# Kernel optimization log

Measured on AMD Instinct MI355X. Metric: run time of the kernel, lower is better.

Reference implementation:

```python
import jax, jax.numpy as jnp
import numpy as np

OBS, ACT, H, B = 128, 32, 64, 32768
TMAX = 8  # max variable-length GRU steps: (15-1)//2+1 == 15//2+1 == 8
CENTER = 7


def gru_last(x_seq, valid, Wih, Whh, bih, bhh):
    """torch nn.GRU cell, masked scan; returns final hidden at each true length.
    x_seq: (B, TMAX, D), valid: (B, TMAX) bool. Gate order r, z, n."""
    Bn = x_seq.shape[0]
    h0 = jnp.zeros((Bn, Whh.shape[1]), x_seq.dtype)

    def step(h, inp):
        xt, vt = inp  # (B, D), (B,)
        gi = xt @ Wih.T + bih
        gh = h @ Whh.T + bhh
        ir, iz, inn = jnp.split(gi, 3, axis=-1)
        hr, hz, hn = jnp.split(gh, 3, axis=-1)
        r = jax.nn.sigmoid(ir + hr)
        zg = jax.nn.sigmoid(iz + hz)
        n = jnp.tanh(inn + r * hn)
        hnew = (1.0 - zg) * n + zg * h
        h = jnp.where(vt[:, None], hnew, h)
        return h, None

    h, _ = jax.lax.scan(step, h0, (jnp.swapaxes(x_seq, 0, 1), valid.T))
    return h


def setup_inputs() -> dict:
    key = jax.random.key(0)
    ks = jax.random.split(key, 20)
    def p(k, shape, s=0.05):
        return jax.random.normal(k, shape, jnp.float32) * s
    D = OBS + ACT
    return dict(
        obs_chunk=jax.random.normal(ks[0], (B, 15, OBS), jnp.float32),
        act_chunk=jax.random.normal(ks[1], (B, 15, ACT), jnp.float32),
        ln_g=jnp.ones((3,), jnp.float32), ln_b=jnp.zeros((3,), jnp.float32),
        dw1=p(ks[2], (16, 3)), db1=jnp.zeros((16,), jnp.float32),
        dw2=p(ks[3], (8, 16)), db2=jnp.zeros((8,), jnp.float32),
        dw3=p(ks[4], (14, 8)), db3=jnp.zeros((14,), jnp.float32),
        Wih_f=p(ks[5], (3 * H, D)), Whh_f=p(ks[6], (3 * H, H)),
        bih_f=jnp.zeros((3 * H,), jnp.float32), bhh_f=jnp.zeros((3 * H,), jnp.float32),
        Wih_b=p(ks[7], (3 * H, D)), Whh_b=p(ks[8], (3 * H, H)),
        bih_b=jnp.zeros((3 * H,), jnp.float32), bhh_b=jnp.zeros((3 * H,), jnp.float32),
        mw1=p(ks[9], (H, 2 * H)), mb1=jnp.zeros((H,), jnp.float32),
        mw2=p(ks[10], (H, H)), mb2=jnp.zeros((H,), jnp.float32),
        mu_w=p(ks[11], (H, H)), mu_b=jnp.zeros((H,), jnp.float32),
        lv_w=p(ks[12], (H, H)), lv_b=jnp.zeros((H,), jnp.float32),
    )


def reference(obs_chunk, act_chunk, ln_g, ln_b, dw1, db1, dw2, db2, dw3, db3,
              Wih_f, Whh_f, bih_f, bhh_f, Wih_b, Whh_b, bih_b, bhh_b,
              mw1, mb1, mw2, mb2, mu_w, mu_b, lv_w, lv_b):
    C = CENTER
    # --- DynamicTimeWindow features ---
    obs_t = obs_chunk[:, C]  # (B, OBS)
    pr = jax.nn.softmax(obs_t, axis=-1)
    entropy = -jnp.sum(pr * jnp.log(pr + 1e-8), axis=-1, keepdims=True)
    diffs = jnp.stack([jnp.linalg.norm(obs_chunk[:, C - k] - obs_chunk[:, C - k - 1], axis=-1)
                       for k in range(3)], axis=1)
    roc = diffs.mean(axis=1, keepdims=True)
    act_prev = act_chunk[:, C - 1]
    md = max(obs_t.shape[-1], act_prev.shape[-1])
    op = jnp.pad(obs_t, ((0, 0), (0, md - obs_t.shape[-1])))
    ap = jnp.pad(act_prev, ((0, 0), (0, md - act_prev.shape[-1])))
    oc = op - op.mean(axis=1, keepdims=True)
    ac = ap - ap.mean(axis=1, keepdims=True)
    denom = (jnp.linalg.norm(oc, axis=1, keepdims=True)
             * jnp.linalg.norm(ac, axis=1, keepdims=True) + 1e-8)
    corr = jnp.sum(oc * ac, axis=1, keepdims=True) / denom
    f = jnp.concatenate([entropy, roc, corr], axis=1)  # (B, 3)
    mean = f.mean(axis=-1, keepdims=True)
    var = f.var(axis=-1, keepdims=True)  # biased, matches torch LayerNorm
    fn = (f - mean) / jnp.sqrt(var + 1e-5) * ln_g + ln_b
    h1 = jax.nn.relu(fn @ dw1.T + db1)
    h2 = jax.nn.relu(h1 @ dw2.T + db2)
    logits = h2 @ dw3.T + db3  # (B, 14)
    widx = jnp.argmax(logits, axis=1)  # test_mode: argmax of softmax == argmax of logits
    wl = widx + 2  # window_len in [2, 15]
    idxs = jnp.arange(15)[None, :]
    start = (C - (wl - 1) // 2)[:, None]
    end = (C + wl // 2 + 1)[:, None]
    mask = ((idxs >= start) & (idxs < end)).astype(obs_chunk.dtype)  # (B, 15)
    x = jnp.concatenate([obs_chunk, act_chunk], axis=-1) * mask[..., None]  # (B, 15, D)
    # --- BiGRU over variable-length windows ---
    len_f = (wl - 1) // 2 + 1  # (B,)
    len_b = wl // 2 + 1
    t = jnp.arange(TMAX)
    idx_f = C - len_f[:, None] + 1 + t[None, :]  # left-aligned forward window
    idx_b = C + len_b[:, None] - 1 - t[None, :]  # reversed backward window
    seq_f = jnp.take_along_axis(x, idx_f[..., None], axis=1)  # (B, 8, D)
    seq_b = jnp.take_along_axis(x, idx_b[..., None], axis=1)
    vf = t[None, :] < len_f[:, None]
    vb = t[None, :] < len_b[:, None]
    h_f = gru_last(seq_f, vf, Wih_f, Whh_f, bih_f, bhh_f)  # (B, H)
    h_b = gru_last(seq_b, vb, Wih_b, Whh_b, bih_b, bhh_b)
    comb = jnp.concatenate([h_f, h_b], axis=1)  # (B, 2H)
    zenc = jax.nn.relu(comb @ mw1.T + mb1) @ mw2.T + mb2
    mu = zenc @ mu_w.T + mu_b
    sigma = jnp.exp(0.5 * (zenc @ lv_w.T + lv_b))
    z = mu  # test_mode=True
    return (z, mu, sigma)
```

## Files before the change

kernel.cpp:

```cpp
#include <hip/hip_runtime.h>

#define OBS 128
#define ACTD 32
#define DIMX 160
#define HID 64
#define NBATCH 32768
#define TMAXX 8
#define CTR 7
#define NPOS 15

typedef short bf16x8 __attribute__((ext_vector_type(8)));
typedef float f32x4 __attribute__((ext_vector_type(4)));

#define MFMA(a,b,c) __builtin_amdgcn_mfma_f32_16x16x32_bf16((a),(b),(c),0,0,0)

#define CTRL_BYTE 262144
#define SIDX_BYTE 278528
#define SIDX_CAP  66560
#define WB_BYTE   544768
#define COMB_BYTE 757760
#define NCB 64
#define EPB 512
#define HEAD_W_OFF 10752
#define TOTAL_SLOTS 13312

__device__ __forceinline__ unsigned short f2bf(float f) {
  unsigned u = __float_as_uint(f);
  return (unsigned short)((u + 0x7FFFu + ((u >> 16) & 1u)) >> 16);
}
__device__ __forceinline__ unsigned cvtpk(float a, float b) {
  unsigned r;
  asm("v_cvt_pk_bf16_f32 %0, %1, %2" : "=v"(r) : "v"(a), "v"(b));
  return r;
}

__device__ __forceinline__ float wsum(float v) {
#pragma unroll
  for (int s = 1; s < 64; s <<= 1) v += __shfl_xor(v, s);
  return v;
}
__device__ __forceinline__ float wmax(float v) {
#pragma unroll
  for (int s = 1; s < 64; s <<= 1) v = fmaxf(v, __shfl_xor(v, s));
  return v;
}

__global__ __launch_bounds__(256) void k_prep(
    const float* __restrict__ Wih_f, const float* __restrict__ Whh_f,
    const float* __restrict__ Wih_b, const float* __restrict__ Whh_b,
    const float* __restrict__ mw1, const float* __restrict__ mw2,
    const float* __restrict__ mu_w, const float* __restrict__ lv_w,
    unsigned short* __restrict__ dst) {
  int slot = blockIdx.x * 256 + threadIdx.x;
  if (slot >= TOTAL_SLOTS) return;
  const float* src;
  if (slot < HEAD_W_OFF) {
    int d = slot / 5376, r = slot % 5376;
    int f = r >> 8, rw = r & 255;
    int w = rw >> 6, lane = rw & 63;
    int col = lane & 15, kgrp = lane >> 4;
    int row = 16 * w + col;
    if (f < 15) {
      int g = f / 5, kf = f % 5;
      const float* W = d ? Wih_b : Wih_f;
      src = W + (size_t)(g * 64 + row) * 160 + kf * 32 + kgrp * 8;
    } else {
      int f2 = f - 15, g = f2 >> 1, kh = f2 & 1;
      const float* W = d ? Whh_b : Whh_f;
      src = W + (size_t)(g * 64 + row) * 64 + kh * 32 + kgrp * 8;
    }
  } else {
    int s2 = slot - HEAD_W_OFF;
    int f = s2 >> 8, rw = s2 & 255;
    int w = rw >> 6, lane = rw & 63;
    int col = lane & 15, kgrp = lane >> 4;
    int gr = 16 * w + col;
    if (f < 4)      src = mw1 + (size_t)gr * 128 + f * 32 + kgrp * 8;
    else if (f < 6) src = mw2 + (size_t)gr * 64 + (f - 4) * 32 + kgrp * 8;
    else if (f < 8) src = mu_w + (size_t)gr * 64 + (f - 6) * 32 + kgrp * 8;
    else            src = lv_w + (size_t)gr * 64 + (f - 8) * 32 + kgrp * 8;
  }
  unsigned short* o = dst + (size_t)slot * 8;
#pragma unroll
  for (int i = 0; i < 8; i++) o[i] = f2bf(src[i]);
}

__global__ __launch_bounds__(256) void k_decide(
    const float* __restrict__ obs, const float* __restrict__ act,
    const float* __restrict__ ln_g, const float* __restrict__ ln_b,
    const float* __restrict__ dw1, const float* __restrict__ db1,
    const float* __restrict__ dw2, const float* __restrict__ db2,
    const float* __restrict__ dw3, const float* __restrict__ db3,
    int* __restrict__ lens) {
  int b = blockIdx.x * 4 + (threadIdx.x >> 6);
  int l = threadIdx.x & 63;
  const float* o7 = obs + ((size_t)b * NPOS + CTR) * OBS;
  const float* o6 = o7 - OBS;
  const float* o5 = o7 - 2 * OBS;
  const float* o4 = o7 - 3 * OBS;
  float x0 = o7[l], x1 = o7[l + 64];
  float y60 = o6[l], y61 = o6[l + 64];
  float y50 = o5[l], y51 = o5[l + 64];
  float y40 = o4[l], y41 = o4[l + 64];
  float ap = (l < 32) ? act[((size_t)b * NPOS + 6) * ACTD + l] : 0.0f;

  float m = wmax(fmaxf(x0, x1));
  float e0 = __expf(x0 - m), e1 = __expf(x1 - m);
  float s = wsum(e0 + e1);
  float dot = wsum(e0 * (x0 - m) + e1 * (x1 - m));
  float ent = __logf(s) - dot / s;

  float d0 = wsum((x0 - y60) * (x0 - y60) + (x1 - y61) * (x1 - y61));
  float d1 = wsum((y60 - y50) * (y60 - y50) + (y61 - y51) * (y61 - y51));
  float d2 = wsum((y50 - y40) * (y50 - y40) + (y51 - y41) * (y51 - y41));
  float roc = (sqrtf(d0) + sqrtf(d1) + sqrtf(d2)) / 3.0f;

  float sop = wsum(x0 + x1);
  float sop2 = wsum(x0 * x0 + x1 * x1);
  float sap = wsum(ap);
  float sap2 = wsum(ap * ap);
  float dotoa = wsum(ap * x0);
  float mo = sop / 128.0f, ma = sap / 128.0f;
  float num = dotoa - 128.0f * mo * ma;
  float oc2 = fmaxf(sop2 - 128.0f * mo * mo, 0.0f);
  float ac2 = fmaxf(sap2 - 128.0f * ma * ma, 0.0f);
  float corr = num / (sqrtf(oc2) * sqrtf(ac2) + 1e-8f);

  float f0 = ent, f1 = roc, f2 = corr;
  float mean = (f0 + f1 + f2) / 3.0f;
  float v0 = f0 - mean, v1 = f1 - mean, v2 = f2 - mean;
  float var = (v0 * v0 + v1 * v1 + v2 * v2) / 3.0f;
  float sd = sqrtf(var + 1e-5f);
  float fn0 = v0 / sd * ln_g[0] + ln_b[0];
  float fn1 = v1 / sd * ln_g[1] + ln_b[1];
  float fn2 = v2 / sd * ln_g[2] + ln_b[2];

  float h1[16];
#pragma unroll
  for (int i = 0; i < 16; i++) {
    float a = db1[i] + fn0 * dw1[i * 3] + fn1 * dw1[i * 3 + 1] + fn2 * dw1[i * 3 + 2];
    h1[i] = fmaxf(a, 0.0f);
  }
  float h2[8];
#pragma unroll
  for (int i = 0; i < 8; i++) {
    float a = db2[i];
#pragma unroll
    for (int j = 0; j < 16; j++) a += h1[j] * dw2[i * 16 + j];
    h2[i] = fmaxf(a, 0.0f);
  }
  float best = -3.0e38f;
  int bi = 0;
#pragma unroll
  for (int i = 0; i < 14; i++) {
    float a = db3[i];
#pragma unroll
    for (int j = 0; j < 8; j++) a += h2[j] * dw3[i * 8 + j];
    if (a > best) { best = a; bi = i; }
  }
  int wl = bi + 2;
  if (l == 0) {
    lens[b] = (wl - 1) / 2 + 1;
    lens[NBATCH + b] = wl / 2 + 1;
  }
}

__global__ __launch_bounds__(256) void k_count(
    const int* __restrict__ lens, int* __restrict__ ctrl) {
  __shared__ int hist[16];
  const int tid = threadIdx.x, blk = blockIdx.x;
  if (tid < 16) hist[tid] = 0;
  __syncthreads();
#pragma unroll
  for (int j = 0; j < 2; j++) {
    int e = blk * EPB + j * 256 + tid;
    atomicAdd(&hist[lens[e] - 1], 1);
    atomicAdd(&hist[8 + lens[NBATCH + e] - 1], 1);
  }
  __syncthreads();
  if (tid < 16) ctrl[32 + 1024 + blk * 16 + tid] = hist[tid];
}

__global__ void k_scan(int* __restrict__ ctrl, int* __restrict__ sidx) {
  __shared__ int tot[16];
  __shared__ int pss[17];
  const int tid = threadIdx.x;
  const int* bh = ctrl + 32 + 1024;
  int* bb = ctrl + 32;
  if (tid < 16) {
    int s = 0;
    for (int blk = 0; blk < NCB; blk++) {
      bb[blk * 16 + tid] = s;
      s += bh[blk * 16 + tid];
    }
    tot[tid] = s;
  }
  __syncthreads();
  if (tid == 0) {
    int acc = 0;
    for (int k = 0; k < 16; k++) {
      pss[k] = acc;
      acc += (tot[k] + 63) & ~63;
    }
    pss[16] = acc;
    for (int k = 0; k < 17; k++) ctrl[k] = pss[k];
  }
  __syncthreads();
  if (tid < 16) {
    for (int blk = 0; blk < NCB; blk++) bb[blk * 16 + tid] += pss[tid];
  }
  __syncthreads();
  for (int k = 0; k < 16; k++) {
    int s = pss[k] + tot[k], e2 = pss[k + 1];
    for (int i = s + tid; i < e2; i += 64) sidx[i] = -1;
  }
}

__global__ __launch_bounds__(256) void k_place(
    const int* __restrict__ lens, const int* __restrict__ ctrl,
    int* __restrict__ sidx) {
  __shared__ int hist[16];
  __shared__ int base[16];
  const int tid = threadIdx.x, blk = blockIdx.x;
  if (tid < 16) {
    hist[tid] = 0;
    base[tid] = ctrl[32 + blk * 16 + tid];
  }
  __syncthreads();
#pragma unroll
  for (int j = 0; j < 2; j++) {
    int e = blk * EPB + j * 256 + tid;
    int binf = lens[e] - 1;
    sidx[base[binf] + atomicAdd(&hist[binf], 1)] = e;
    int binb = 8 + lens[NBATCH + e] - 1;
    sidx[base[binb] + atomicAdd(&hist[binb], 1)] = e;
  }
}

__global__ __launch_bounds__(256, 2) void k_gru(
    const float* __restrict__ obs, const float* __restrict__ act,
    const int* __restrict__ ctrl, const int* __restrict__ sidx,
    const unsigned short* __restrict__ wbf,
    const float* __restrict__ bih_f, const float* __restrict__ bhh_f,
    const float* __restrict__ bih_b, const float* __restrict__ bhh_b,
    unsigned short* __restrict__ comb) {
  __shared__ unsigned short Xl[2][64 * 168];
  __shared__ unsigned short Hl[2][64 * 72];
  __shared__ int ei[64];

  const int tid = threadIdx.x;
  const int p = blockIdx.x * 64;
  const int* ps = ctrl;
  if (p >= ps[16]) return;
  int bin = 0;
#pragma unroll
  for (int k = 1; k < 16; k++) bin += (p >= ps[k]) ? 1 : 0;
  const int d = bin >> 3;
  const int len = (bin & 7) + 1;

  if (tid < 64) ei[tid] = sidx[p + tid];
  __syncthreads();

  const int w = tid >> 6, l = tid & 63;
  const int col = l & 15, kgrp = l >> 4;
  const int gr = 16 * w + col;

  const float* bih = d ? bih_b : bih_f;
  const float* bhh = d ? bhh_b : bhh_f;
  const float bias_r = bih[gr] + bhh[gr];
  const float bias_z = bih[64 + gr] + bhh[64 + gr];
  const float bias_in = bih[128 + gr];
  const float bias_hn = bhh[128 + gr];

  const unsigned short* fb = wbf + ((size_t)d * 5376 + tid) * 8;
  bf16x8 wr[5], wz[5], wn[5];
#pragma unroll
  for (int kf = 0; kf < 5; kf++) {
    wr[kf] = *(const bf16x8*)(fb + (size_t)kf * 2048);
    wz[kf] = *(const bf16x8*)(fb + (size_t)(5 + kf) * 2048);
    wn[kf] = *(const bf16x8*)(fb + (size_t)(10 + kf) * 2048);
  }
  bf16x8 vr[2], vz[2], vn[2];
#pragma unroll
  for (int kh = 0; kh < 2; kh++) {
    vr[kh] = *(const bf16x8*)(fb + (size_t)(15 + kh) * 2048);
    vz[kh] = *(const bf16x8*)(fb + (size_t)(17 + kh) * 2048);
    vn[kh] = *(const bf16x8*)(fb + (size_t)(19 + kh) * 2048);
  }

  const int p0 = d ? (CTR + len - 1) : (CTR - len + 1);
  int soff[10];
  int sdo[10];
  unsigned qmask = 0;
#pragma unroll
  for (int it = 0; it < 10; it++) {
    int i = tid + it * 256;
    int eloc = i / 40;
    int q = i - eloc * 40;
    int eg = ei[eloc];
    if (eg < 0) eg = ei[0];
    if (q < 32) {
      soff[it] = eg * (NPOS * OBS) + p0 * OBS + q * 4;
      qmask |= 1u << it;
      sdo[it] = eloc * 168 + q * 4;
    } else {
      soff[it] = eg * (NPOS * ACTD) + p0 * ACTD + (q - 32) * 4;
      sdo[it] = eloc * 168 + 128 + (q - 32) * 4;
    }
  }
  const int sA = d ? -OBS : OBS;
  const int sB = d ? -ACTD : ACTD;
  float4 sv[10];

  auto stage_issue = [&](int t1) {
    int offA = t1 * sA, offB = t1 * sB;
#pragma unroll
    for (int it = 0; it < 10; it++) {
      bool isObs = (qmask >> it) & 1u;
      const float* bp = isObs ? obs : act;
      int o = soff[it] + (isObs ? offA : offB);
      sv[it] = *(const float4*)(bp + o);
    }
  };
  auto stage_commit = [&](int buf) {
#pragma unroll
    for (int it = 0; it < 10; it++) {
      uint2 pk;
      pk.x = cvtpk(sv[it].x, sv[it].y);
      pk.y = cvtpk(sv[it].z, sv[it].w);
      *(uint2*)(&Xl[buf][sdo[it]]) = pk;
    }
  };

  stage_issue(0);
  stage_commit(0);
  __syncthreads();

  f32x4 hreg[4];
#pragma unroll
  for (int m = 0; m < 4; m++) hreg[m] = (f32x4){0.f, 0.f, 0.f, 0.f};

  for (int t = 0; t < len; t++) {
    const int cur = t & 1, nxt = cur ^ 1;
    const bool more = (t + 1 < len);
    if (more) stage_issue(t + 1);

#pragma unroll
    for (int m = 0; m < 4; m++) {
      f32x4 ar = (f32x4){0.f, 0.f, 0.f, 0.f};
      f32x4 az = (f32x4){0.f, 0.f, 0.f, 0.f};
      f32x4 ain = (f32x4){0.f, 0.f, 0.f, 0.f};
      f32x4 ahn = (f32x4){0.f, 0.f, 0.f, 0.f};
#pragma unroll
      for (int kf = 0; kf < 5; kf++) {
        bf16x8 xa = *(const bf16x8*)(&Xl[cur][(col + 16 * m) * 168 + kf * 32 + kgrp * 8]);
        ar = MFMA(xa, wr[kf], ar);
        az = MFMA(xa, wz[kf], az);
        ain = MFMA(xa, wn[kf], ain);
      }
      if (t > 0) {
#pragma unroll
        for (int kh = 0; kh < 2; kh++) {
          bf16x8 ha = *(const bf16x8*)(&Hl[cur][(col + 16 * m) * 72 + kh * 32 + kgrp * 8]);
          ar = MFMA(ha, vr[kh], ar);
          az = MFMA(ha, vz[kh], az);
          ahn = MFMA(ha, vn[kh], ahn);
        }
      }
      float hvv[4];
#pragma unroll
      for (int r = 0; r < 4; r++) {
        float air = ar[r] + bias_r;
        float aiz = az[r] + bias_z;
        float rg = __builtin_amdgcn_rcpf(1.0f + __expf(-air));
        float zg = __builtin_amdgcn_rcpf(1.0f + __expf(-aiz));
        float nn = fmaf(rg, ahn[r] + bias_hn, ain[r] + bias_in);
        float th = fmaf(-2.0f, __builtin_amdgcn_rcpf(__expf(2.0f * nn) + 1.0f), 1.0f);
        float hp = hreg[m][r];
        float hv = fmaf(zg, hp - th, th);
        hreg[m][r] = hv;
        hvv[r] = hv;
      }
      if (more) {
        unsigned ua = cvtpk(hvv[0], hvv[1]);
        unsigned ub = cvtpk(hvv[2], hvv[3]);
        int row0 = (16 * m + kgrp * 4) * 72 + gr;
        Hl[nxt][row0] = (unsigned short)ua;
        Hl[nxt][row0 + 72] = (unsigned short)(ua >> 16);
        Hl[nxt][row0 + 144] = (unsigned short)ub;
        Hl[nxt][row0 + 216] = (unsigned short)(ub >> 16);
      }
    }

    if (more) {
      stage_commit(nxt);
      __syncthreads();
    }
  }

#pragma unroll
  for (int m = 0; m < 4; m++) {
#pragma unroll
    for (int r = 0; r < 4; r++) {
      int eg = ei[16 * m + kgrp * 4 + r];
      if (eg >= 0)
        comb[(size_t)eg * 128 + 64 * d + gr] = f2bf(hreg[m][r]);
    }
  }
}

__global__ __launch_bounds__(256) void k_head(
    const unsigned short* __restrict__ comb, const unsigned short* __restrict__ wbf,
    const float* __restrict__ mb1, const float* __restrict__ mb2,
    const float* __restrict__ mu_b, const float* __restrict__ lv_b,
    float* __restrict__ out) {
  __shared__ unsigned short Cl[64 * 136];
  __shared__ unsigned short Hl[64 * 72];
  __shared__ unsigned short Zl[64 * 72];

  const int tid = threadIdx.x;
  const int w = tid >> 6, l = tid & 63;
  const int col = l & 15, kgrp = l >> 4;
  const int gr = 16 * w + col;
  const int base = blockIdx.x * 64;

  {
    int row = tid >> 2, sq = tid & 3;
    const uint4* src = (const uint4*)(comb + (size_t)(base + row) * 128 + sq * 32);
    uint4* dst = (uint4*)(&Cl[row * 136 + sq * 32]);
#pragma unroll
    for (int j = 0; j < 4; j++) dst[j] = src[j];
  }
  __syncthreads();

  const unsigned short* hfb = wbf + ((size_t)HEAD_W_OFF + tid) * 8;
  const float b1 = mb1[gr], b2v = mb2[gr], bmu = mu_b[gr], blv = lv_b[gr];

  f32x4 t1[4];
#pragma unroll
  for (int m = 0; m < 4; m++) t1[m] = (f32x4){0.f, 0.f, 0.f, 0.f};
#pragma unroll
  for (int kf = 0; kf < 4; kf++) {
    bf16x8 bw = *(const bf16x8*)(hfb + (size_t)kf * 2048);
#pragma unroll
    for (int m = 0; m < 4; m++) {
      bf16x8 ca = *(const bf16x8*)(&Cl[(col + 16 * m) * 136 + kf * 32 + kgrp * 8]);
      t1[m] = MFMA(ca, bw, t1[m]);
    }
  }
#pragma unroll
  for (int m = 0; m < 4; m++) {
#pragma unroll
    for (int r = 0; r < 4; r++) {
      float v = fmaxf(t1[m][r] + b1, 0.0f);
      Hl[(16 * m + kgrp * 4 + r) * 72 + gr] = f2bf(v);
    }
  }
  __syncthreads();

  f32x4 ze[4];
#pragma unroll
  for (int m = 0; m < 4; m++) ze[m] = (f32x4){0.f, 0.f, 0.f, 0.f};
#pragma unroll
  for (int kh = 0; kh < 2; kh++) {
    bf16x8 bw = *(const bf16x8*)(hfb + (size_t)(4 + kh) * 2048);
#pragma unroll
    for (int m = 0; m < 4; m++) {
      bf16x8 ha = *(const bf16x8*)(&Hl[(col + 16 * m) * 72 + kh * 32 + kgrp * 8]);
      ze[m] = MFMA(ha, bw, ze[m]);
    }
  }
#pragma unroll
  for (int m = 0; m < 4; m++) {
#pragma unroll
    for (int r = 0; r < 4; r++) {
      Zl[(16 * m + kgrp * 4 + r) * 72 + gr] = f2bf(ze[m][r] + b2v);
    }
  }
  __syncthreads();

  f32x4 amu[4], alv[4];
#pragma unroll
  for (int m = 0; m < 4; m++) {
    amu[m] = (f32x4){0.f, 0.f, 0.f, 0.f};
    alv[m] = (f32x4){0.f, 0.f, 0.f, 0.f};
  }
#pragma unroll
  for (int kh = 0; kh < 2; kh++) {
    bf16x8 bwm = *(const bf16x8*)(hfb + (size_t)(6 + kh) * 2048);
    bf16x8 bwl = *(const bf16x8*)(hfb + (size_t)(8 + kh) * 2048);
#pragma unroll
    for (int m = 0; m < 4; m++) {
      bf16x8 za = *(const bf16x8*)(&Zl[(col + 16 * m) * 72 + kh * 32 + kgrp * 8]);
      amu[m] = MFMA(za, bwm, amu[m]);
      alv[m] = MFMA(za, bwl, alv[m]);
    }
  }
#pragma unroll
  for (int m = 0; m < 4; m++) {
#pragma unroll
    for (int r = 0; r < 4; r++) {
      int e = 16 * m + kgrp * 4 + r;
      float mu = amu[m][r] + bmu;
      float sg = expf(0.5f * (alv[m][r] + blv));
      size_t o = (size_t)(base + e) * HID + gr;
      out[o] = mu;
      out[(size_t)NBATCH * HID + o] = mu;
      out[2 * (size_t)NBATCH * HID + o] = sg;
    }
  }
}

extern "C" void kernel_launch(void* const* d_in, const int* in_sizes, int n_in,
                              void* d_out, int out_size, void* d_ws, size_t ws_size,
                              hipStream_t stream) {
  const float* obs = (const float*)d_in[0];
  const float* act = (const float*)d_in[1];
  const float* ln_g = (const float*)d_in[2];
  const float* ln_b = (const float*)d_in[3];
  const float* dw1 = (const float*)d_in[4];
  const float* db1 = (const float*)d_in[5];
  const float* dw2 = (const float*)d_in[6];
  const float* db2 = (const float*)d_in[7];
  const float* dw3 = (const float*)d_in[8];
  const float* db3 = (const float*)d_in[9];
  const float* Wih_f = (const float*)d_in[10];
  const float* Whh_f = (const float*)d_in[11];
  const float* bih_f = (const float*)d_in[12];
  const float* bhh_f = (const float*)d_in[13];
  const float* Wih_b = (const float*)d_in[14];
  const float* Whh_b = (const float*)d_in[15];
  const float* bih_b = (const float*)d_in[16];
  const float* bhh_b = (const float*)d_in[17];
  const float* mw1 = (const float*)d_in[18];
  const float* mb1 = (const float*)d_in[19];
  const float* mw2 = (const float*)d_in[20];
  const float* mb2 = (const float*)d_in[21];
  const float* mu_w = (const float*)d_in[22];
  const float* mu_b = (const float*)d_in[23];
  const float* lv_w = (const float*)d_in[24];
  const float* lv_b = (const float*)d_in[25];

  int* lens = (int*)d_ws;
  int* ctrl = (int*)((char*)d_ws + CTRL_BYTE);
  int* sidx = (int*)((char*)d_ws + SIDX_BYTE);
  unsigned short* wbf = (unsigned short*)((char*)d_ws + WB_BYTE);
  unsigned short* comb = (unsigned short*)((char*)d_ws + COMB_BYTE);

  k_prep<<<(TOTAL_SLOTS + 255) / 256, 256, 0, stream>>>(
      Wih_f, Whh_f, Wih_b, Whh_b, mw1, mw2, mu_w, lv_w, wbf);
  k_decide<<<NBATCH / 4, 256, 0, stream>>>(obs, act, ln_g, ln_b, dw1, db1, dw2,
                                           db2, dw3, db3, lens);
  k_count<<<NCB, 256, 0, stream>>>(lens, ctrl);
  k_scan<<<1, 64, 0, stream>>>(ctrl, sidx);
  k_place<<<NCB, 256, 0, stream>>>(lens, ctrl, sidx);
  k_gru<<<SIDX_CAP / 64, 256, 0, stream>>>(obs, act, ctrl, sidx, wbf, bih_f,
                                           bhh_f, bih_b, bhh_b, comb);
  k_head<<<NBATCH / 64, 256, 0, stream>>>(comb, wbf, mb1, mb2, mu_b, lv_b,
                                          (float*)d_out);
}
```

Baseline: 133.9 us.

## Halve GRU tile to 32 rows, pad bins to 32, order bins longest-first

Result: slower. 161.4 us (+20.6%).

```diff
diff --git a/kernel.cpp b/kernel.cpp
--- a/kernel.cpp
+++ b/kernel.cpp
@@ -16,11 +16,13 @@
 
 #define CTRL_BYTE 262144
 #define SIDX_BYTE 278528
-#define SIDX_CAP  66560
-#define WB_BYTE   544768
-#define COMB_BYTE 757760
+#define SIDX_CAP  66048
+#define WB_BYTE   542720
+#define COMB_BYTE 755712
 #define NCB 64
 #define EPB 512
+#define BB_OFF 40
+#define BH_OFF (40 + 1024)
 #define HEAD_W_OFF 10752
 #define TOTAL_SLOTS 13312
 
@@ -178,15 +180,17 @@
     atomicAdd(&hist[8 + lens[NBATCH + e] - 1], 1);
   }
   __syncthreads();
-  if (tid < 16) ctrl[32 + 1024 + blk * 16 + tid] = hist[tid];
+  if (tid < 16) ctrl[BH_OFF + blk * 16 + tid] = hist[tid];
 }
 
 __global__ void k_scan(int* __restrict__ ctrl, int* __restrict__ sidx) {
   __shared__ int tot[16];
   __shared__ int pss[17];
+  __shared__ int border[16];
+  __shared__ int bstart[16];
   const int tid = threadIdx.x;
-  const int* bh = ctrl + 32 + 1024;
-  int* bb = ctrl + 32;
+  const int* bh = ctrl + BH_OFF;
+  int* bb = ctrl + BB_OFF;
   if (tid < 16) {
     int s = 0;
     for (int blk = 0; blk < NCB; blk++) {
@@ -198,20 +202,25 @@
   __syncthreads();
   if (tid == 0) {
     int acc = 0;
-    for (int k = 0; k < 16; k++) {
-      pss[k] = acc;
-      acc += (tot[k] + 63) & ~63;
+    for (int r = 0; r < 16; r++) {
+      int bin = (r & 1) * 8 + 7 - (r >> 1);
+      border[r] = bin;
+      pss[r] = acc;
+      bstart[bin] = acc;
+      acc += (tot[bin] + 31) & ~31;
     }
     pss[16] = acc;
-    for (int k = 0; k < 17; k++) ctrl[k] = pss[k];
+    for (int r = 0; r < 17; r++) ctrl[r] = pss[r];
+    for (int r = 0; r < 16; r++) ctrl[17 + r] = border[r];
   }
   __syncthreads();
   if (tid < 16) {
-    for (int blk = 0; blk < NCB; blk++) bb[blk * 16 + tid] += pss[tid];
-  }
-  __syncthreads();
-  for (int k = 0; k < 16; k++) {
-    int s = pss[k] + tot[k], e2 = pss[k + 1];
+    for (int blk = 0; blk < NCB; blk++) bb[blk * 16 + tid] += bstart[tid];
+  }
+  __syncthreads();
+  for (int r = 0; r < 16; r++) {
+    int bin = border[r];
+    int s = pss[r] + tot[bin], e2 = pss[r + 1];
     for (int i = s + tid; i < e2; i += 64) sidx[i] = -1;
   }
 }
@@ -224,7 +233,7 @@
   const int tid = threadIdx.x, blk = blockIdx.x;
   if (tid < 16) {
     hist[tid] = 0;
-    base[tid] = ctrl[32 + blk * 16 + tid];
+    base[tid] = ctrl[BB_OFF + blk * 16 + tid];
   }
   __syncthreads();
 #pragma unroll
@@ -237,28 +246,28 @@
   }
 }
 
-__global__ __launch_bounds__(256, 2) void k_gru(
+__global__ __launch_bounds__(256, 3) void k_gru(
     const float* __restrict__ obs, const float* __restrict__ act,
     const int* __restrict__ ctrl, const int* __restrict__ sidx,
     const unsigned short* __restrict__ wbf,
     const float* __restrict__ bih_f, const float* __restrict__ bhh_f,
     const float* __restrict__ bih_b, const float* __restrict__ bhh_b,
     unsigned short* __restrict__ comb) {
-  __shared__ unsigned short Xl[2][64 * 168];
-  __shared__ unsigned short Hl[2][64 * 72];
-  __shared__ int ei[64];
+  __shared__ unsigned short Xl[2][32 * 168];
+  __shared__ unsigned short Hl[2][32 * 72];
+  __shared__ int ei[32];
 
   const int tid = threadIdx.x;
-  const int p = blockIdx.x * 64;
-  const int* ps = ctrl;
-  if (p >= ps[16]) return;
-  int bin = 0;
-#pragma unroll
-  for (int k = 1; k < 16; k++) bin += (p >= ps[k]) ? 1 : 0;
+  const int p = blockIdx.x * 32;
+  if (p >= ctrl[16]) return;
+  int r = 0;
+#pragma unroll
+  for (int k = 1; k < 16; k++) r += (p >= ctrl[k]) ? 1 : 0;
+  const int bin = ctrl[17 + r];
   const int d = bin >> 3;
   const int len = (bin & 7) + 1;
 
-  if (tid < 64) ei[tid] = sidx[p + tid];
+  if (tid < 32) ei[tid] = sidx[p + tid];
   __syncthreads();
 
   const int w = tid >> 6, l = tid & 63;
@@ -289,11 +298,10 @@
   }
 
   const int p0 = d ? (CTR + len - 1) : (CTR - len + 1);
-  int soff[10];
-  int sdo[10];
+  int soff[5];
   unsigned qmask = 0;
 #pragma unroll
-  for (int it = 0; it < 10; it++) {
+  for (int it = 0; it < 5; it++) {
     int i = tid + it * 256;
     int eloc = i / 40;
     int q = i - eloc * 40;
@@ -302,33 +310,34 @@
     if (q < 32) {
       soff[it] = eg * (NPOS * OBS) + p0 * OBS + q * 4;
       qmask |= 1u << it;
-      sdo[it] = eloc * 168 + q * 4;
     } else {
       soff[it] = eg * (NPOS * ACTD) + p0 * ACTD + (q - 32) * 4;
-      sdo[it] = eloc * 168 + 128 + (q - 32) * 4;
     }
   }
   const int sA = d ? -OBS : OBS;
   const int sB = d ? -ACTD : ACTD;
-  float4 sv[10];
+  float4 sv[5];
 
   auto stage_issue = [&](int t1) {
     int offA = t1 * sA, offB = t1 * sB;
 #pragma unroll
-    for (int it = 0; it < 10; it++) {
+    for (int it = 0; it < 5; it++) {
       bool isObs = (qmask >> it) & 1u;
       const float* bp = isObs ? obs : act;
-      int o = soff[it] + (isObs ? offA : offB);
-      sv[it] = *(const float4*)(bp + o);
+      sv[it] = *(const float4*)(bp + soff[it] + (isObs ? offA : offB));
     }
   };
   auto stage_commit = [&](int buf) {
 #pragma unroll
-    for (int it = 0; it < 10; it++) {
+    for (int it = 0; it < 5; it++) {
+      int i = tid + it * 256;
+      int eloc = i / 40;
+      int q = i - eloc * 40;
+      int sdo = eloc * 168 + ((q < 32) ? q * 4 : 128 + (q - 32) * 4);
       uint2 pk;
       pk.x = cvtpk(sv[it].x, sv[it].y);
       pk.y = cvtpk(sv[it].z, sv[it].w);
-      *(uint2*)(&Xl[buf][sdo[it]]) = pk;
+      *(uint2*)(&Xl[buf][sdo]) = pk;
     }
   };
 
@@ -336,9 +345,9 @@
   stage_commit(0);
   __syncthreads();
 
-  f32x4 hreg[4];
-#pragma unroll
-  for (int m = 0; m < 4; m++) hreg[m] = (f32x4){0.f, 0.f, 0.f, 0.f};
+  f32x4 hreg[2];
+#pragma unroll
+  for (int m = 0; m < 2; m++) hreg[m] = (f32x4){0.f, 0.f, 0.f, 0.f};
 
   for (int t = 0; t < len; t++) {
     const int cur = t & 1, nxt = cur ^ 1;
@@ -346,7 +355,7 @@
     if (more) stage_issue(t + 1);
 
 #pragma unroll
-    for (int m = 0; m < 4; m++) {
+    for (int m = 0; m < 2; m++) {
       f32x4 ar = (f32x4){0.f, 0.f, 0.f, 0.f};
       f32x4 az = (f32x4){0.f, 0.f, 0.f, 0.f};
       f32x4 ain = (f32x4){0.f, 0.f, 0.f, 0.f};
@@ -369,17 +378,17 @@
       }
       float hvv[4];
 #pragma unroll
-      for (int r = 0; r < 4; r++) {
-        float air = ar[r] + bias_r;
-        float aiz = az[r] + bias_z;
+      for (int r2 = 0; r2 < 4; r2++) {
+        float air = ar[r2] + bias_r;
+        float aiz = az[r2] + bias_z;
         float rg = __builtin_amdgcn_rcpf(1.0f + __expf(-air));
         float zg = __builtin_amdgcn_rcpf(1.0f + __expf(-aiz));
-        float nn = fmaf(rg, ahn[r] + bias_hn, ain[r] + bias_in);
+        float nn = fmaf(rg, ahn[r2] + bias_hn, ain[r2] + bias_in);
         float th = fmaf(-2.0f, __builtin_amdgcn_rcpf(__expf(2.0f * nn) + 1.0f), 1.0f);
-        float hp = hreg[m][r];
+        float hp = hreg[m][r2];
         float hv = fmaf(zg, hp - th, th);
-        hreg[m][r] = hv;
-        hvv[r] = hv;
+        hreg[m][r2] = hv;
+        hvv[r2] = hv;
       }
       if (more) {
         unsigned ua = cvtpk(hvv[0], hvv[1]);
@@ -399,12 +408,12 @@
   }
 
 #pragma unroll
-  for (int m = 0; m < 4; m++) {
-#pragma unroll
-    for (int r = 0; r < 4; r++) {
-      int eg = ei[16 * m + kgrp * 4 + r];
+  for (int m = 0; m < 2; m++) {
+#pragma unroll
+    for (int r2 = 0; r2 < 4; r2++) {
+      int eg = ei[16 * m + kgrp * 4 + r2];
       if (eg >= 0)
-        comb[(size_t)eg * 128 + 64 * d + gr] = f2bf(hreg[m][r]);
+        comb[(size_t)eg * 128 + 64 * d + gr] = f2bf(hreg[m][r2]);
     }
   }
 }
@@ -554,7 +563,7 @@
   k_count<<<NCB, 256, 0, stream>>>(lens, ctrl);
   k_scan<<<1, 64, 0, stream>>>(ctrl, sidx);
   k_place<<<NCB, 256, 0, stream>>>(lens, ctrl, sidx);
-  k_gru<<<SIDX_CAP / 64, 256, 0, stream>>>(obs, act, ctrl, sidx, wbf, bih_f,
+  k_gru<<<SIDX_CAP / 32, 256, 0, stream>>>(obs, act, ctrl, sidx, wbf, bih_f,
                                            bhh_f, bih_b, bhh_b, comb);
   k_head<<<NBATCH / 64, 256, 0, stream>>>(comb, wbf, mb1, mb2, mu_b, lv_b,
                                           (float*)d_out);
```
